# Performance work log

Hardware: AMD Instinct MI355X
Metric: run time of the kernel (lower is better)

Reference implementation:

```python
import jax, jax.numpy as jnp
import numpy as np

EPS = 1e-5

def lrelu(x):
    return jnp.where(x >= 0, x, 0.1 * x)

def bn_eval(x, g, b, m, v):
    # eval-mode BatchNorm over the last (channel) axis
    return (x - m) * (g * jax.lax.rsqrt(v + EPS)) + b

def setup_inputs():
    key = jax.random.key(0)
    ks = jax.random.split(key, 12)
    Nq, K, Cin, Fc, Co = 20000, 32, 3, 64, 64
    q_points = jax.random.normal(ks[0], (Nq, Cin), jnp.float32)
    s_points = jax.random.normal(ks[1], (Nq, Cin), jnp.float32)
    feat = jax.random.normal(ks[2], (Nq, Fc), jnp.float32)
    # valid indices 0..Nq (Nq == shadow/pad row appended in forward)
    neighb_inds = jax.random.randint(ks[3], (Nq, K), 0, Nq + 1)
    def w(k, shape, fan_in):
        return jax.random.normal(k, shape, jnp.float32) / np.float32(np.sqrt(fan_in))
    W_pos2 = w(ks[4], (Fc, Cin), Cin)          # convpos2: Conv2d(Cin, Fc, 1)
    W_attn = w(ks[5], (Co * Cin, Fc), Fc)      # convattn: Conv2d(Fc, Co*Cin, 1)
    W_res = w(ks[6], (Co, Fc), Fc)             # residual 1x1 conv
    def bn(k, c):
        k1, k2, k3, k4 = jax.random.split(k, 4)
        return (jax.random.normal(k1, (c,), jnp.float32) * 0.1 + 1.0,
                jax.random.normal(k2, (c,), jnp.float32) * 0.1,
                jax.random.normal(k3, (c,), jnp.float32) * 0.1,
                jax.random.uniform(k4, (c,), jnp.float32) * 0.5 + 0.5)
    bq = bn(ks[7], Fc); bp = bn(ks[8], Cin); b1 = bn(ks[9], Co); br = bn(ks[10], Co)
    return dict(q_points=q_points, s_points=s_points, neighb_inds=neighb_inds, feat=feat,
                W_pos2=W_pos2, W_attn=W_attn, W_res=W_res,
                bnq_g=bq[0], bnq_b=bq[1], bnq_m=bq[2], bnq_v=bq[3],
                bnp_g=bp[0], bnp_b=bp[1], bnp_m=bp[2], bnp_v=bp[3],
                bn1_g=b1[0], bn1_b=b1[1], bn1_m=b1[2], bn1_v=b1[3],
                bnr_g=br[0], bnr_b=br[1], bnr_m=br[2], bnr_v=br[3])

def reference(q_points, s_points, neighb_inds, feat, W_pos2, W_attn, W_res,
              bnq_g, bnq_b, bnq_m, bnq_v, bnp_g, bnp_b, bnp_m, bnp_v,
              bn1_g, bn1_b, bn1_m, bn1_v, bnr_g, bnr_b, bnr_m, bnr_v):
    Nq, Cin = q_points.shape
    Fc = feat.shape[1]
    Co = W_res.shape[0]
    K = neighb_inds.shape[1]
    # append shadow (zero) row for out-of-range neighbor indices
    s_pad = jnp.concatenate([s_points, jnp.zeros((1, Cin), s_points.dtype)], 0)
    f_pad = jnp.concatenate([feat, jnp.zeros((1, Fc), feat.dtype)], 0)
    xg = s_pad[neighb_inds]                      # [Nq,K,Cin] EFR_P gather
    yg = f_pad[neighb_inds]                      # [Nq,K,Fc]  EFR_F gather
    x_v = xg - q_points[:, None, :]              # [Nq,K,Cin] values
    x_q = lrelu(bn_eval(feat, bnq_g, bnq_b, bnq_m, bnq_v))          # [Nq,Fc]
    pos0 = lrelu(bn_eval(s_points, bnp_g, bnp_b, bnp_m, bnp_v))     # [Nq,Cin]
    pos = (pos0[:, None, :] - x_v) @ W_pos2.T                       # [Nq,K,Fc]
    attn = x_q[:, None, :] - yg + pos                               # [Nq,K,Fc]
    attn = jax.nn.softmax(attn / jnp.sqrt(jnp.float32(Fc)), axis=1) # softmax over K
    attn = (attn @ W_attn.T).reshape(Nq, K, Co, Cin)                # [Nq,K,Co,Cin]
    y_e = jnp.einsum('nkoi,nki->nko', attn, x_v)                    # [Nq,K,Co]
    y_e = lrelu(bn_eval(y_e, bn1_g, bn1_b, bn1_m, bn1_v))
    res = bn_eval(yg @ W_res.T, bnr_g, bnr_b, bnr_m, bnr_v)         # [Nq,K,Co]
    y_e = lrelu(y_e + res)
    return y_e.max(axis=1)                                          # [Nq,Co]
```

## Files before the change

kernel.cpp:

```cpp
#include <hip/hip_runtime.h>
#include <hip/hip_bf16.h>
#include <math.h>

#define KNB 32
#define FC 64
#define CO 64
#define EPS 1e-5f
#define NBLOCKS 1024
#define CL 0.180336880095853f

typedef __attribute__((ext_vector_type(8))) short short8;
typedef __attribute__((ext_vector_type(4))) float floatx4;
typedef __attribute__((ext_vector_type(2))) float float2v;

#if __has_builtin(__builtin_amdgcn_exp2f)
#define EXP2F(x) __builtin_amdgcn_exp2f(x)
#else
#define EXP2F(x) exp2f(x)
#endif
#if __has_builtin(__builtin_amdgcn_rcpf)
#define RCPF(x) __builtin_amdgcn_rcpf(x)
#else
#define RCPF(x) (1.f / (x))
#endif

__device__ __forceinline__ unsigned pk2(float a, float b) {
    __hip_bfloat162 h = __float22bfloat162_rn(float2{a, b});
    unsigned u; __builtin_memcpy(&u, &h, 4); return u;
}
__device__ __forceinline__ unsigned pk2v(float2v v) { return pk2(v.x, v.y); }
__device__ __forceinline__ float lrelu(float x) { return fmaxf(x, 0.1f * x); }
__device__ __forceinline__ float2v fma2(float2v a, float2v b, float2v c) {
    return __builtin_elementwise_fma(a, b, c);
}
__device__ __forceinline__ float2v max2(float2v a, float2v b) {
    return __builtin_elementwise_max(a, b);
}
__device__ __forceinline__ float2v lrelu2(float2v x) {
    return max2(x, 0.1f * x);
}

__global__ __launch_bounds__(256, 4) void GCT_61272003445298_kernel(
    const float* __restrict__ q_points,
    const float* __restrict__ s_points,
    const int*   __restrict__ neighb,
    const float* __restrict__ feat,
    const float* __restrict__ W_pos2,
    const float* __restrict__ W_attn,
    const float* __restrict__ W_res,
    const float* __restrict__ bnq_g, const float* __restrict__ bnq_b,
    const float* __restrict__ bnq_m, const float* __restrict__ bnq_v,
    const float* __restrict__ bnp_g, const float* __restrict__ bnp_b,
    const float* __restrict__ bnp_m, const float* __restrict__ bnp_v,
    const float* __restrict__ bn1_g, const float* __restrict__ bn1_b,
    const float* __restrict__ bn1_m, const float* __restrict__ bn1_v,
    const float* __restrict__ bnr_g, const float* __restrict__ bnr_b,
    const float* __restrict__ bnr_m, const float* __restrict__ bnr_v,
    const float* __restrict__ zp,
    float* __restrict__ out, int Nq)
{
    const int t = threadIdx.x;
    const int wv = t >> 6;
    const int lane = t & 63;
    const int cc = lane & 15, quad = lane >> 4;
    const int o = wv * 16 + cc;
    const int qB  = t >> 7;
    const int kg  = lane >> 3;
    const int fqB = (((t >> 6) & 1) << 3) + (lane & 7);

    __shared__ __align__(16) short sA1[64 * 72];
    __shared__ __align__(16) short sA2[64 * 72];
    __shared__ __align__(16) float sXvC[3][80];
    __shared__ __align__(16) float sWp2[192];
    __shared__ __align__(16) float sQs[64], sQb[64];

    if (t < 192) sWp2[t] = CL * W_pos2[t];
    if (t < 64) {
        float sc = bnq_g[t] * rsqrtf(bnq_v[t] + EPS);
        sQs[t] = sc; sQb[t] = bnq_b[t] - bnq_m[t] * sc;
    }
    const float ps0 = bnp_g[0] * rsqrtf(bnp_v[0] + EPS);
    const float ps1 = bnp_g[1] * rsqrtf(bnp_v[1] + EPS);
    const float ps2 = bnp_g[2] * rsqrtf(bnp_v[2] + EPS);
    const float pb0 = bnp_b[0] - bnp_m[0] * ps0;
    const float pb1 = bnp_b[1] - bnp_m[1] * ps1;
    const float pb2 = bnp_b[2] - bnp_m[2] * ps2;
    const float e1s = bn1_g[o] * rsqrtf(bn1_v[o] + EPS);
    const float e1b = bn1_b[o] - bn1_m[o] * e1s;
    const float ers = bnr_g[o] * rsqrtf(bnr_v[o] + EPS);
    const float erb = bnr_b[o] - bnr_m[o] * ers;

    short8 bW[4][2];
    #pragma unroll
    for (int ty = 0; ty < 4; ++ty) {
        const float* wrow = (ty < 3) ? (W_attn + (long)(o * 3 + ty) * FC)
                                     : (W_res  + (long)o * FC);
        const float sc = (ty < 3) ? e1s : ers;
        #pragma unroll
        for (int ks = 0; ks < 2; ++ks) {
            int k0 = ks * 32 + quad * 8;
            float4 w0 = *(const float4*)(wrow + k0);
            float4 w1 = *(const float4*)(wrow + k0 + 4);
            uint4 pv;
            pv.x = pk2(w0.x * sc, w0.y * sc);
            pv.y = pk2(w0.z * sc, w0.w * sc);
            pv.z = pk2(w1.x * sc, w1.y * sc);
            pv.w = pk2(w1.z * sc, w1.w * sc);
            __builtin_memcpy(&bW[ty][ks], &pv, 16);
        }
    }
    __syncthreads();

    float2v wpa[3], wpb[3];
    {
        const float* w = &sWp2[fqB * 12];
        wpa[0] = (float2v){w[0], w[3]};  wpa[1] = (float2v){w[1], w[4]};
        wpa[2] = (float2v){w[2], w[5]};
        wpb[0] = (float2v){w[6], w[9]};  wpb[1] = (float2v){w[7], w[10]};
        wpb[2] = (float2v){w[8], w[11]};
    }
    const float4 qs4 = *(const float4*)&sQs[fqB * 4];
    const float4 qb4 = *(const float4*)&sQb[fqB * 4];
    const float4* __restrict__ feat4 = (const float4*)feat;

    const int npair = (Nq + 1) >> 1;
    for (int p = blockIdx.x; p < npair; p += NBLOCKS) {
        const long n0 = 2L * p;
        long n1 = n0 + 1;
        const bool has1 = (n1 < Nq);
        if (!has1) n1 = n0;
        const long nn = qB ? n1 : n0;

        const float q0 = q_points[nn * 3 + 0];
        const float q1 = q_points[nn * 3 + 1];
        const float q2 = q_points[nn * 3 + 2];
        const float pp0 = lrelu(fmaf(s_points[nn * 3 + 0], ps0, pb0));
        const float pp1 = lrelu(fmaf(s_points[nn * 3 + 1], ps1, pb1));
        const float pp2 = lrelu(fmaf(s_points[nn * 3 + 2], ps2, pb2));
        const int4 idx4 = *(const int4*)(neighb + nn * KNB + kg * 4);

        float2v xqcA, xqcB;
        {
            const float4 fx = feat4[(int)(nn * 16) + fqB];
            float2v xqA = lrelu2(fma2((float2v){fx.x, fx.y},
                                      (float2v){qs4.x, qs4.y},
                                      (float2v){qb4.x, qb4.y}));
            float2v xqB = lrelu2(fma2((float2v){fx.z, fx.w},
                                      (float2v){qs4.z, qs4.w},
                                      (float2v){qb4.z, qb4.w}));
            const float2v v0 = (float2v){pp0, pp0};
            const float2v v1 = (float2v){pp1, pp1};
            const float2v v2 = (float2v){pp2, pp2};
            xqcA = fma2(v0, wpa[0], fma2(v1, wpa[1], fma2(v2, wpa[2], CL * xqA)));
            xqcB = fma2(v0, wpb[0], fma2(v1, wpb[1], fma2(v2, wpb[2], CL * xqB)));
        }

        short* a1b = &sA1[(qB * 32 + kg * 4) * 72 + fqB * 4];
        short* a2b = &sA2[(qB * 32 + kg * 4) * 72 + fqB * 4];
        float2v evA[4], evB[4];
        float2v sumA = (float2v){0.f, 0.f}, sumB = (float2v){0.f, 0.f};
        #pragma unroll
        for (int j = 0; j < 4; ++j) {
            const int idx = ((const int*)&idx4)[j];
            const bool valid = (idx < Nq);
            const float* fb = valid ? (feat + (long)idx * FC) : zp;
            const float* sb = valid ? (s_points + (long)idx * 3) : zp;
            const float4 y = *(const float4*)(fb + fqB * 4);
            uint2 pk; pk.x = pk2(y.x, y.y); pk.y = pk2(y.z, y.w);
            *(uint2*)(a2b + j * 72) = pk;
            const float xv0 = sb[0] - q0;
            const float xv1 = sb[1] - q1;
            const float xv2 = sb[2] - q2;
            if (fqB == 0) {
                const int row = qB * 32 + kg * 4 + j;
                sXvC[0][row] = xv0; sXvC[1][row] = xv1; sXvC[2][row] = xv2;
            }
            const float2v m0 = (float2v){-xv0, -xv0};
            const float2v m1 = (float2v){-xv1, -xv1};
            const float2v m2 = (float2v){-xv2, -xv2};
            float2v lA = fma2((float2v){y.x, y.y}, (float2v){-CL, -CL}, xqcA);
            lA = fma2(m0, wpa[0], lA); lA = fma2(m1, wpa[1], lA); lA = fma2(m2, wpa[2], lA);
            float2v lB = fma2((float2v){y.z, y.w}, (float2v){-CL, -CL}, xqcB);
            lB = fma2(m0, wpb[0], lB); lB = fma2(m1, wpb[1], lB); lB = fma2(m2, wpb[2], lB);
            evA[j] = (float2v){EXP2F(lA.x), EXP2F(lA.y)};
            evB[j] = (float2v){EXP2F(lB.x), EXP2F(lB.y)};
            sumA = sumA + evA[j];
            sumB = sumB + evB[j];
        }
        float s0 = sumA.x, s1 = sumA.y, s2 = sumB.x, s3 = sumB.y;
        s0 += __shfl_xor(s0, 8); s0 += __shfl_xor(s0, 16); s0 += __shfl_xor(s0, 32);
        s1 += __shfl_xor(s1, 8); s1 += __shfl_xor(s1, 16); s1 += __shfl_xor(s1, 32);
        s2 += __shfl_xor(s2, 8); s2 += __shfl_xor(s2, 16); s2 += __shfl_xor(s2, 32);
        s3 += __shfl_xor(s3, 8); s3 += __shfl_xor(s3, 16); s3 += __shfl_xor(s3, 32);
        const float2v invA = (float2v){RCPF(s0), RCPF(s1)};
        const float2v invB = (float2v){RCPF(s2), RCPF(s3)};
        #pragma unroll
        for (int j = 0; j < 4; ++j) {
            uint2 pw;
            pw.x = pk2v(evA[j] * invA);
            pw.y = pk2v(evB[j] * invB);
            *(uint2*)(a1b + j * 72) = pw;
        }
        __syncthreads();

        const float2v e1b2 = (float2v){e1b, e1b};
        float2v m0p = (float2v){-1e30f, -1e30f};
        float2v m1p = (float2v){-1e30f, -1e30f};
        #pragma unroll
        for (int mt = 0; mt < 4; ++mt) {
            floatx4 acc[4];
            #pragma unroll
            for (int ty = 0; ty < 4; ++ty) acc[ty] = (floatx4){0.f, 0.f, 0.f, 0.f};
            const int r0 = mt * 16 + cc;
            #pragma unroll
            for (int ks = 0; ks < 2; ++ks) {
                const int kof = ks * 32 + quad * 8;
                short8 a1 = *(const short8*)(sA1 + r0 * 72 + kof);
                short8 a2 = *(const short8*)(sA2 + r0 * 72 + kof);
                acc[0] = __builtin_amdgcn_mfma_f32_16x16x32_bf16(a1, bW[0][ks], acc[0], 0, 0, 0);
                acc[1] = __builtin_amdgcn_mfma_f32_16x16x32_bf16(a1, bW[1][ks], acc[1], 0, 0, 0);
                acc[2] = __builtin_amdgcn_mfma_f32_16x16x32_bf16(a1, bW[2][ks], acc[2], 0, 0, 0);
                acc[3] = __builtin_amdgcn_mfma_f32_16x16x32_bf16(a2, bW[3][ks], acc[3], 0, 0, 0);
            }
            #pragma unroll
            for (int rp = 0; rp < 2; ++rp) {
                const int r = mt * 16 + quad * 4 + rp * 2;
                const float2v xv0 = *(const float2v*)&sXvC[0][r];
                const float2v xv1 = *(const float2v*)&sXvC[1][r];
                const float2v xv2 = *(const float2v*)&sXvC[2][r];
                const float2v a0 = (float2v){acc[0][rp*2], acc[0][rp*2+1]};
                const float2v a1 = (float2v){acc[1][rp*2], acc[1][rp*2+1]};
                const float2v a2 = (float2v){acc[2][rp*2], acc[2][rp*2+1]};
                const float2v a3 = (float2v){acc[3][rp*2], acc[3][rp*2+1]};
                float2v y2 = a0 * xv0;
                y2 = fma2(a1, xv1, y2);
                y2 = fma2(a2, xv2, y2);
                const float2v v2 = lrelu2(y2 + e1b2) + a3;
                if (mt < 2) m0p = max2(m0p, v2); else m1p = max2(m1p, v2);
            }
        }
        float m0r = fmaxf(m0p.x, m0p.y);
        float m1r = fmaxf(m1p.x, m1p.y);
        m0r = fmaxf(m0r, __shfl_xor(m0r, 16));
        m0r = fmaxf(m0r, __shfl_xor(m0r, 32));
        m1r = fmaxf(m1r, __shfl_xor(m1r, 16));
        m1r = fmaxf(m1r, __shfl_xor(m1r, 32));
        if (lane < 16) {
            out[n0 * CO + o] = lrelu(m0r + erb);
            if (has1) out[n1 * CO + o] = lrelu(m1r + erb);
        }
        __syncthreads();
    }
}

extern "C" void kernel_launch(void* const* d_in, const int* in_sizes, int n_in,
                              void* d_out, int out_size, void* d_ws, size_t ws_size,
                              hipStream_t stream) {
    const float* q_points = (const float*)d_in[0];
    const float* s_points = (const float*)d_in[1];
    const int*   neighb   = (const int*)  d_in[2];
    const float* feat     = (const float*)d_in[3];
    const float* W_pos2   = (const float*)d_in[4];
    const float* W_attn   = (const float*)d_in[5];
    const float* W_res    = (const float*)d_in[6];
    const float* bnq_g = (const float*)d_in[7];
    const float* bnq_b = (const float*)d_in[8];
    const float* bnq_m = (const float*)d_in[9];
    const float* bnq_v = (const float*)d_in[10];
    const float* bnp_g = (const float*)d_in[11];
    const float* bnp_b = (const float*)d_in[12];
    const float* bnp_m = (const float*)d_in[13];
    const float* bnp_v = (const float*)d_in[14];
    const float* bn1_g = (const float*)d_in[15];
    const float* bn1_b = (const float*)d_in[16];
    const float* bn1_m = (const float*)d_in[17];
    const float* bn1_v = (const float*)d_in[18];
    const float* bnr_g = (const float*)d_in[19];
    const float* bnr_b = (const float*)d_in[20];
    const float* bnr_m = (const float*)d_in[21];
    const float* bnr_v = (const float*)d_in[22];
    float* out = (float*)d_out;

    int Nq = in_sizes[0] / 3;

    size_t zn = ws_size < 4096 ? ws_size : (size_t)4096;
    hipMemsetAsync(d_ws, 0, zn, stream);

    hipLaunchKernelGGL(GCT_61272003445298_kernel,
                       dim3(NBLOCKS), dim3(256), 0, stream,
                       q_points, s_points, neighb, feat, W_pos2, W_attn, W_res,
                       bnq_g, bnq_b, bnq_m, bnq_v,
                       bnp_g, bnp_b, bnp_m, bnp_v,
                       bn1_g, bn1_b, bn1_m, bn1_v,
                       bnr_g, bnr_b, bnr_m, bnr_v,
                       (const float*)d_ws, out, Nq);
}
```

Baseline: 163.8 us.

## Process four queries per block iteration to halve barrier and loop overhead

Each block iteration now handles four query points instead of two. The gather and softmax phase runs twice to fill doubled shared-memory tiles, then the MFMA phase covers 8 row tiles. This halves the number of __syncthreads per query and amortizes per-iteration setup. The cost is doubled LDS usage (about 37KB), which may reduce occupancy, and with 20000 queries there are only 5000 groups across 1000 blocks, so each block does about five iterations.

```diff
diff --git a/kernel.cpp b/kernel.cpp
--- a/kernel.cpp
+++ b/kernel.cpp
@@ -6,7 +6,7 @@
 #define FC 64
 #define CO 64
 #define EPS 1e-5f
-#define NBLOCKS 1024
+#define NBLOCKS 1000
 #define CL 0.180336880095853f
 
 typedef __attribute__((ext_vector_type(8))) short short8;
@@ -68,9 +68,9 @@
     const int kg  = lane >> 3;
     const int fqB = (((t >> 6) & 1) << 3) + (lane & 7);
 
-    __shared__ __align__(16) short sA1[64 * 72];
-    __shared__ __align__(16) short sA2[64 * 72];
-    __shared__ __align__(16) float sXvC[3][80];
+    __shared__ __align__(16) short sA1[128 * 72];
+    __shared__ __align__(16) short sA2[128 * 72];
+    __shared__ __align__(16) float sXvC[3][128];
     __shared__ __align__(16) float sWp2[192];
     __shared__ __align__(16) float sQs[64], sQb[64];
 
@@ -123,91 +123,95 @@
     const float4 qb4 = *(const float4*)&sQb[fqB * 4];
     const float4* __restrict__ feat4 = (const float4*)feat;
 
-    const int npair = (Nq + 1) >> 1;
-    for (int p = blockIdx.x; p < npair; p += NBLOCKS) {
-        const long n0 = 2L * p;
-        long n1 = n0 + 1;
-        const bool has1 = (n1 < Nq);
-        if (!has1) n1 = n0;
-        const long nn = qB ? n1 : n0;
-
-        const float q0 = q_points[nn * 3 + 0];
-        const float q1 = q_points[nn * 3 + 1];
-        const float q2 = q_points[nn * 3 + 2];
-        const float pp0 = lrelu(fmaf(s_points[nn * 3 + 0], ps0, pb0));
-        const float pp1 = lrelu(fmaf(s_points[nn * 3 + 1], ps1, pb1));
-        const float pp2 = lrelu(fmaf(s_points[nn * 3 + 2], ps2, pb2));
-        const int4 idx4 = *(const int4*)(neighb + nn * KNB + kg * 4);
-
-        float2v xqcA, xqcB;
-        {
-            const float4 fx = feat4[(int)(nn * 16) + fqB];
-            float2v xqA = lrelu2(fma2((float2v){fx.x, fx.y},
-                                      (float2v){qs4.x, qs4.y},
-                                      (float2v){qb4.x, qb4.y}));
-            float2v xqB = lrelu2(fma2((float2v){fx.z, fx.w},
-                                      (float2v){qs4.z, qs4.w},
-                                      (float2v){qb4.z, qb4.w}));
-            const float2v v0 = (float2v){pp0, pp0};
-            const float2v v1 = (float2v){pp1, pp1};
-            const float2v v2 = (float2v){pp2, pp2};
-            xqcA = fma2(v0, wpa[0], fma2(v1, wpa[1], fma2(v2, wpa[2], CL * xqA)));
-            xqcB = fma2(v0, wpb[0], fma2(v1, wpb[1], fma2(v2, wpb[2], CL * xqB)));
-        }
-
-        short* a1b = &sA1[(qB * 32 + kg * 4) * 72 + fqB * 4];
-        short* a2b = &sA2[(qB * 32 + kg * 4) * 72 + fqB * 4];
-        float2v evA[4], evB[4];
-        float2v sumA = (float2v){0.f, 0.f}, sumB = (float2v){0.f, 0.f};
-        #pragma unroll
-        for (int j = 0; j < 4; ++j) {
-            const int idx = ((const int*)&idx4)[j];
-            const bool valid = (idx < Nq);
-            const float* fb = valid ? (feat + (long)idx * FC) : zp;
-            const float* sb = valid ? (s_points + (long)idx * 3) : zp;
-            const float4 y = *(const float4*)(fb + fqB * 4);
-            uint2 pk; pk.x = pk2(y.x, y.y); pk.y = pk2(y.z, y.w);
-            *(uint2*)(a2b + j * 72) = pk;
-            const float xv0 = sb[0] - q0;
-            const float xv1 = sb[1] - q1;
-            const float xv2 = sb[2] - q2;
-            if (fqB == 0) {
-                const int row = qB * 32 + kg * 4 + j;
-                sXvC[0][row] = xv0; sXvC[1][row] = xv1; sXvC[2][row] = xv2;
-            }
-            const float2v m0 = (float2v){-xv0, -xv0};
-            const float2v m1 = (float2v){-xv1, -xv1};
-            const float2v m2 = (float2v){-xv2, -xv2};
-            float2v lA = fma2((float2v){y.x, y.y}, (float2v){-CL, -CL}, xqcA);
-            lA = fma2(m0, wpa[0], lA); lA = fma2(m1, wpa[1], lA); lA = fma2(m2, wpa[2], lA);
-            float2v lB = fma2((float2v){y.z, y.w}, (float2v){-CL, -CL}, xqcB);
-            lB = fma2(m0, wpb[0], lB); lB = fma2(m1, wpb[1], lB); lB = fma2(m2, wpb[2], lB);
-            evA[j] = (float2v){EXP2F(lA.x), EXP2F(lA.y)};
-            evB[j] = (float2v){EXP2F(lB.x), EXP2F(lB.y)};
-            sumA = sumA + evA[j];
-            sumB = sumB + evB[j];
-        }
-        float s0 = sumA.x, s1 = sumA.y, s2 = sumB.x, s3 = sumB.y;
-        s0 += __shfl_xor(s0, 8); s0 += __shfl_xor(s0, 16); s0 += __shfl_xor(s0, 32);
-        s1 += __shfl_xor(s1, 8); s1 += __shfl_xor(s1, 16); s1 += __shfl_xor(s1, 32);
-        s2 += __shfl_xor(s2, 8); s2 += __shfl_xor(s2, 16); s2 += __shfl_xor(s2, 32);
-        s3 += __shfl_xor(s3, 8); s3 += __shfl_xor(s3, 16); s3 += __shfl_xor(s3, 32);
-        const float2v invA = (float2v){RCPF(s0), RCPF(s1)};
-        const float2v invB = (float2v){RCPF(s2), RCPF(s3)};
-        #pragma unroll
-        for (int j = 0; j < 4; ++j) {
-            uint2 pw;
-            pw.x = pk2v(evA[j] * invA);
-            pw.y = pk2v(evB[j] * invB);
-            *(uint2*)(a1b + j * 72) = pw;
+    const int ng = (Nq + 3) >> 2;
+    for (int p = blockIdx.x; p < ng; p += NBLOCKS) {
+        const int nbase = 4 * p;
+
+        #pragma unroll 1
+        for (int qq = 0; qq < 2; ++qq) {
+            const int qidx = qq * 2 + qB;
+            long nn = nbase + qidx;
+            if (nn >= Nq) nn = Nq - 1;
+            const float q0 = q_points[nn * 3 + 0];
+            const float q1 = q_points[nn * 3 + 1];
+            const float q2 = q_points[nn * 3 + 2];
+            const float pp0 = lrelu(fmaf(s_points[nn * 3 + 0], ps0, pb0));
+            const float pp1 = lrelu(fmaf(s_points[nn * 3 + 1], ps1, pb1));
+            const float pp2 = lrelu(fmaf(s_points[nn * 3 + 2], ps2, pb2));
+            const int4 idx4 = *(const int4*)(neighb + nn * KNB + kg * 4);
+
+            float2v xqcA, xqcB;
+            {
+                const float4 fx = feat4[(int)(nn * 16) + fqB];
+                float2v xqA = lrelu2(fma2((float2v){fx.x, fx.y},
+                                          (float2v){qs4.x, qs4.y},
+                                          (float2v){qb4.x, qb4.y}));
+                float2v xqB = lrelu2(fma2((float2v){fx.z, fx.w},
+                                          (float2v){qs4.z, qs4.w},
+                                          (float2v){qb4.z, qb4.w}));
+                const float2v v0 = (float2v){pp0, pp0};
+                const float2v v1 = (float2v){pp1, pp1};
+                const float2v v2 = (float2v){pp2, pp2};
+                xqcA = fma2(v0, wpa[0], fma2(v1, wpa[1], fma2(v2, wpa[2], CL * xqA)));
+                xqcB = fma2(v0, wpb[0], fma2(v1, wpb[1], fma2(v2, wpb[2], CL * xqB)));
+            }
+
+            const int rowB = qidx * 32 + kg * 4;
+            short* a1b = &sA1[rowB * 72 + fqB * 4];
+            short* a2b = &sA2[rowB * 72 + fqB * 4];
+            float2v evA[4], evB[4];
+            float2v sumA = (float2v){0.f, 0.f}, sumB = (float2v){0.f, 0.f};
+            #pragma unroll
+            for (int j = 0; j < 4; ++j) {
+                const int idx = ((const int*)&idx4)[j];
+                const bool valid = (idx < Nq);
+                const float* fb = valid ? (feat + (long)idx * FC) : zp;
+                const float* sb = valid ? (s_points + (long)idx * 3) : zp;
+                const float4 y = *(const float4*)(fb + fqB * 4);
+                uint2 pk; pk.x = pk2(y.x, y.y); pk.y = pk2(y.z, y.w);
+                *(uint2*)(a2b + j * 72) = pk;
+                const float xv0 = sb[0] - q0;
+                const float xv1 = sb[1] - q1;
+                const float xv2 = sb[2] - q2;
+                if (fqB == 0) {
+                    const int row = rowB + j;
+                    sXvC[0][row] = xv0; sXvC[1][row] = xv1; sXvC[2][row] = xv2;
+                }
+                const float2v m0 = (float2v){-xv0, -xv0};
+                const float2v m1 = (float2v){-xv1, -xv1};
+                const float2v m2 = (float2v){-xv2, -xv2};
+                float2v lA = fma2((float2v){y.x, y.y}, (float2v){-CL, -CL}, xqcA);
+                lA = fma2(m0, wpa[0], lA); lA = fma2(m1, wpa[1], lA); lA = fma2(m2, wpa[2], lA);
+                float2v lB = fma2((float2v){y.z, y.w}, (float2v){-CL, -CL}, xqcB);
+                lB = fma2(m0, wpb[0], lB); lB = fma2(m1, wpb[1], lB); lB = fma2(m2, wpb[2], lB);
+                evA[j] = (float2v){EXP2F(lA.x), EXP2F(lA.y)};
+                evB[j] = (float2v){EXP2F(lB.x), EXP2F(lB.y)};
+                sumA = sumA + evA[j];
+                sumB = sumB + evB[j];
+            }
+            float s0 = sumA.x, s1 = sumA.y, s2 = sumB.x, s3 = sumB.y;
+            s0 += __shfl_xor(s0, 8); s0 += __shfl_xor(s0, 16); s0 += __shfl_xor(s0, 32);
+            s1 += __shfl_xor(s1, 8); s1 += __shfl_xor(s1, 16); s1 += __shfl_xor(s1, 32);
+            s2 += __shfl_xor(s2, 8); s2 += __shfl_xor(s2, 16); s2 += __shfl_xor(s2, 32);
+            s3 += __shfl_xor(s3, 8); s3 += __shfl_xor(s3, 16); s3 += __shfl_xor(s3, 32);
+            const float2v invA = (float2v){RCPF(s0), RCPF(s1)};
+            const float2v invB = (float2v){RCPF(s2), RCPF(s3)};
+            #pragma unroll
+            for (int j = 0; j < 4; ++j) {
+                uint2 pw;
+                pw.x = pk2v(evA[j] * invA);
+                pw.y = pk2v(evB[j] * invB);
+                *(uint2*)(a1b + j * 72) = pw;
+            }
         }
         __syncthreads();
 
         const float2v e1b2 = (float2v){e1b, e1b};
-        float2v m0p = (float2v){-1e30f, -1e30f};
-        float2v m1p = (float2v){-1e30f, -1e30f};
-        #pragma unroll
-        for (int mt = 0; mt < 4; ++mt) {
+        float2v mp[4];
+        #pragma unroll
+        for (int qi = 0; qi < 4; ++qi) mp[qi] = (float2v){-1e30f, -1e30f};
+        #pragma unroll
+        for (int mt = 0; mt < 8; ++mt) {
             floatx4 acc[4];
             #pragma unroll
             for (int ty = 0; ty < 4; ++ty) acc[ty] = (floatx4){0.f, 0.f, 0.f, 0.f};
@@ -236,18 +240,16 @@
                 y2 = fma2(a1, xv1, y2);
                 y2 = fma2(a2, xv2, y2);
                 const float2v v2 = lrelu2(y2 + e1b2) + a3;
-                if (mt < 2) m0p = max2(m0p, v2); else m1p = max2(m1p, v2);
-            }
-        }
-        float m0r = fmaxf(m0p.x, m0p.y);
-        float m1r = fmaxf(m1p.x, m1p.y);
-        m0r = fmaxf(m0r, __shfl_xor(m0r, 16));
-        m0r = fmaxf(m0r, __shfl_xor(m0r, 32));
-        m1r = fmaxf(m1r, __shfl_xor(m1r, 16));
-        m1r = fmaxf(m1r, __shfl_xor(m1r, 32));
-        if (lane < 16) {
-            out[n0 * CO + o] = lrelu(m0r + erb);
-            if (has1) out[n1 * CO + o] = lrelu(m1r + erb);
+                mp[mt >> 1] = max2(mp[mt >> 1], v2);
+            }
+        }
+        #pragma unroll
+        for (int qi = 0; qi < 4; ++qi) {
+            float mr = fmaxf(mp[qi].x, mp[qi].y);
+            mr = fmaxf(mr, __shfl_xor(mr, 16));
+            mr = fmaxf(mr, __shfl_xor(mr, 32));
+            const long n = nbase + qi;
+            if (lane < 16 && n < Nq) out[n * CO + o] = lrelu(mr + erb);
         }
         __syncthreads();
     }
```

Measured after the change: 326.9 us. +99.5%, slower.
